# Kernel optimization log

Hardware: AMD Instinct MI355X
Metric: run time of the kernel (lower is better)

Reference implementation:

```python
import jax, jax.numpy as jnp
import numpy as np

DIM = 384
NUM_BLOCKS = 3
BATCH = 1024

def setup_inputs() -> dict:
    key = jax.random.key(0)
    k1, k2, kW, kL = jax.random.split(key, 4)
    v1 = jax.random.normal(k1, (BATCH, DIM), dtype=jnp.float32)
    v2 = jax.random.normal(k2, (BATCH, DIM), dtype=jnp.float32)
    block_W = jax.random.normal(kW, (NUM_BLOCKS, DIM, DIM), dtype=jnp.float32) * 0.02
    block_b = jnp.zeros((NUM_BLOCKS, DIM, DIM), dtype=jnp.float32)
    row_weights = jnp.ones((DIM,), dtype=jnp.float32) / DIM
    lim = 1.0 / np.sqrt(DIM)
    kLw, kLb = jax.random.split(kL)
    lin_W = jax.random.uniform(kLw, (DIM, DIM), minval=-lim, maxval=lim, dtype=jnp.float32)
    lin_b = jax.random.uniform(kLb, (DIM,), minval=-lim, maxval=lim, dtype=jnp.float32)
    return {"v1": v1, "v2": v2, "block_W": block_W, "block_b": block_b,
            "row_weights": row_weights, "lin_W": lin_W, "lin_b": lin_b}

def reference(v1, v2, block_W, block_b, row_weights, lin_W, lin_b):
    # outer product: (B, D, D)
    M = v1[:, :, None] * v2[:, None, :]
    for i in range(block_W.shape[0]):
        # M - (M*W + b) = M*(1 - W) - b, fused elementwise affine
        M = M * (1.0 - block_W[i]) - block_b[i]
    pooled = jnp.einsum('i,bij->bj', row_weights, M)
    # nn.Linear: x @ W.T + b
    return pooled @ lin_W.T + lin_b
```

## Files before the change

kernel.cpp:

```cpp
#include <hip/hip_runtime.h>
#include <hip/hip_bf16.h>

#define DIM 384
#define BATCH 1024
#define SPLANE (DIM * DIM)

__device__ __forceinline__ unsigned tobf(float x) {
    unsigned u = __float_as_uint(x);
    return (u + 0x7fffu + ((u >> 16) & 1u)) >> 16;
}
__device__ __forceinline__ float bflo(unsigned u) {
    return __uint_as_float(u << 16);
}
__device__ __forceinline__ float bfhi(unsigned u) {
    return __uint_as_float(u & 0xffff0000u);
}

__global__ __launch_bounds__(128)
void prep_kernel(const float* __restrict__ W,
                 const float* __restrict__ Bb,
                 const float* __restrict__ rw,
                 unsigned* __restrict__ Prwp,
                 float* __restrict__ qc) {
    const int j  = blockIdx.x * 128 + threadIdx.x;
    const int i0 = blockIdx.y * 6;
    float s = 0.0f;
    float p[6];
    #pragma unroll
    for (int ii = 0; ii < 6; ++ii) {
        const int i = i0 + ii;
        const int idx = i * DIM + j;
        float w0 = W[idx], w1 = W[SPLANE + idx], w2 = W[2 * SPLANE + idx];
        float b0 = Bb[idx], b1 = Bb[SPLANE + idx], b2 = Bb[2 * SPLANE + idx];
        float r1 = 1.0f - w1, r2 = 1.0f - w2;
        float r = rw[i];
        p[ii] = r * (1.0f - w0) * r1 * r2;
        s += r * (b0 * r1 * r2 + b1 * r2 + b2);
    }
    #pragma unroll
    for (int t = 0; t < 3; ++t) {
        unsigned lo = tobf(p[2 * t]);
        unsigned hi = tobf(p[2 * t + 1]);
        Prwp[(3 * blockIdx.y + t) * DIM + j] = lo | (hi << 16);
    }
    atomicAdd(&qc[j], s);
}

__global__ __launch_bounds__(256)
void tconv_kernel(const float* __restrict__ Wl,
                  unsigned* __restrict__ Wtp) {
    __shared__ float T[64][65];
    const int n0 = blockIdx.x * 64;
    const int j0 = blockIdx.y * 64;
    const int tid = threadIdx.x;
    const int c  = tid & 63;
    const int r4 = tid >> 6;
    #pragma unroll
    for (int q = 0; q < 16; ++q) {
        int row = r4 + 4 * q;
        T[row][c] = Wl[(n0 + row) * DIM + j0 + c];
    }
    __syncthreads();
    #pragma unroll
    for (int q = 0; q < 8; ++q) {
        int jp = r4 + 4 * q;
        unsigned lo = tobf(T[c][2 * jp]);
        unsigned hi = tobf(T[c][2 * jp + 1]);
        Wtp[(j0 / 2 + jp) * DIM + n0 + c] = lo | (hi << 16);
    }
}

__global__ __launch_bounds__(384)
void fused_kernel(const float* __restrict__ v1,
                  const float* __restrict__ v2,
                  const unsigned* __restrict__ Prwp,
                  const unsigned* __restrict__ Wtp,
                  const float* __restrict__ qc,
                  const float* __restrict__ lb,
                  float* __restrict__ out) {
    __shared__ float AT[DIM][4];
    __shared__ float PT[DIM][4];
    const int bm  = blockIdx.x * 4;
    const int tid = threadIdx.x;

    {
        const int r  = tid & 3;
        const int kq = tid >> 2;
        float4 a = *(const float4*)&v1[(bm + r) * DIM + 4 * kq];
        AT[4 * kq + 0][r] = a.x;
        AT[4 * kq + 1][r] = a.y;
        AT[4 * kq + 2][r] = a.z;
        AT[4 * kq + 3][r] = a.w;
    }
    __syncthreads();

    float a0 = 0.f, a1 = 0.f, a2 = 0.f, a3 = 0.f;
    {
        const unsigned* bp = Prwp + tid;
        #pragma unroll 8
        for (int kp = 0; kp < DIM / 2; ++kp) {
            unsigned u = bp[kp * DIM];
            float blo = bflo(u), bhi = bfhi(u);
            float4 va = *(const float4*)&AT[2 * kp][0];
            float4 vb = *(const float4*)&AT[2 * kp + 1][0];
            a0 += va.x * blo + vb.x * bhi;
            a1 += va.y * blo + vb.y * bhi;
            a2 += va.z * blo + vb.z * bhi;
            a3 += va.w * blo + vb.w * bhi;
        }
    }
    {
        float q = qc[tid];
        float4 pv;
        pv.x = v2[(bm + 0) * DIM + tid] * a0 - q;
        pv.y = v2[(bm + 1) * DIM + tid] * a1 - q;
        pv.z = v2[(bm + 2) * DIM + tid] * a2 - q;
        pv.w = v2[(bm + 3) * DIM + tid] * a3 - q;
        *(float4*)&PT[tid][0] = pv;
    }
    __syncthreads();

    float o0 = 0.f, o1 = 0.f, o2 = 0.f, o3 = 0.f;
    {
        const unsigned* wp = Wtp + tid;
        #pragma unroll 8
        for (int jp = 0; jp < DIM / 2; ++jp) {
            unsigned u = wp[jp * DIM];
            float wlo = bflo(u), whi = bfhi(u);
            float4 pa = *(const float4*)&PT[2 * jp][0];
            float4 pb = *(const float4*)&PT[2 * jp + 1][0];
            o0 += pa.x * wlo + pb.x * whi;
            o1 += pa.y * wlo + pb.y * whi;
            o2 += pa.z * wlo + pb.z * whi;
            o3 += pa.w * wlo + pb.w * whi;
        }
    }
    {
        float b = lb[tid];
        out[(bm + 0) * DIM + tid] = o0 + b;
        out[(bm + 1) * DIM + tid] = o1 + b;
        out[(bm + 2) * DIM + tid] = o2 + b;
        out[(bm + 3) * DIM + tid] = o3 + b;
    }
}

extern "C" void kernel_launch(void* const* d_in, const int* in_sizes, int n_in,
                              void* d_out, int out_size, void* d_ws, size_t ws_size,
                              hipStream_t stream) {
    const float* v1  = (const float*)d_in[0];
    const float* v2  = (const float*)d_in[1];
    const float* bW  = (const float*)d_in[2];
    const float* bB  = (const float*)d_in[3];
    const float* rw  = (const float*)d_in[4];
    const float* lW  = (const float*)d_in[5];
    const float* lb  = (const float*)d_in[6];
    float* out = (float*)d_out;

    float*    qc   = (float*)d_ws;
    unsigned* Prwp = (unsigned*)((char*)d_ws + 4096);
    unsigned* Wtp  = Prwp + (DIM / 2) * DIM;

    hipMemsetAsync(qc, 0, DIM * sizeof(float), stream);

    dim3 gp(DIM / 128, DIM / 6);
    prep_kernel<<<gp, 128, 0, stream>>>(bW, bB, rw, Prwp, qc);

    dim3 gt(DIM / 64, DIM / 64);
    tconv_kernel<<<gt, 256, 0, stream>>>(lW, Wtp);

    fused_kernel<<<BATCH / 4, 384, 0, stream>>>(v1, v2, Prwp, Wtp, qc, lb, out);
}
```

Baseline: 99.83 us.

## Merge prep kernels, drop memset and atomics, widen bf16 weight loads to uint2

Combines the block-weight precompute and the linear-weight transpose/convert into one launch, and removes the memset plus atomicAdd by writing per-block partial bias sums that the main kernel reduces itself. Weights are repacked as four bf16 values per uint2, so the GEMV loops issue half as many global loads, each twice as wide. This trades two launches and a memset for a 96-element partial-sum reduction inside every fused block.

Result: no change. 101.6 us (+1.8%).

```diff
diff --git a/kernel.cpp b/kernel.cpp
--- a/kernel.cpp
+++ b/kernel.cpp
@@ -9,73 +9,73 @@
     unsigned u = __float_as_uint(x);
     return (u + 0x7fffu + ((u >> 16) & 1u)) >> 16;
 }
-__device__ __forceinline__ float bflo(unsigned u) {
-    return __uint_as_float(u << 16);
-}
-__device__ __forceinline__ float bfhi(unsigned u) {
-    return __uint_as_float(u & 0xffff0000u);
-}
+__device__ __forceinline__ float bflo(unsigned u) { return __uint_as_float(u << 16); }
+__device__ __forceinline__ float bfhi(unsigned u) { return __uint_as_float(u & 0xffff0000u); }
 
-__global__ __launch_bounds__(128)
-void prep_kernel(const float* __restrict__ W,
-                 const float* __restrict__ Bb,
-                 const float* __restrict__ rw,
-                 unsigned* __restrict__ Prwp,
-                 float* __restrict__ qc) {
-    const int j  = blockIdx.x * 128 + threadIdx.x;
-    const int i0 = blockIdx.y * 6;
-    float s = 0.0f;
-    float p[6];
-    #pragma unroll
-    for (int ii = 0; ii < 6; ++ii) {
-        const int i = i0 + ii;
-        const int idx = i * DIM + j;
-        float w0 = W[idx], w1 = W[SPLANE + idx], w2 = W[2 * SPLANE + idx];
-        float b0 = Bb[idx], b1 = Bb[SPLANE + idx], b2 = Bb[2 * SPLANE + idx];
-        float r1 = 1.0f - w1, r2 = 1.0f - w2;
-        float r = rw[i];
-        p[ii] = r * (1.0f - w0) * r1 * r2;
-        s += r * (b0 * r1 * r2 + b1 * r2 + b2);
-    }
-    #pragma unroll
-    for (int t = 0; t < 3; ++t) {
-        unsigned lo = tobf(p[2 * t]);
-        unsigned hi = tobf(p[2 * t + 1]);
-        Prwp[(3 * blockIdx.y + t) * DIM + j] = lo | (hi << 16);
-    }
-    atomicAdd(&qc[j], s);
-}
+__global__ __launch_bounds__(384)
+void prep_all(const float* __restrict__ W,
+              const float* __restrict__ Bb,
+              const float* __restrict__ rw,
+              const float* __restrict__ Wl,
+              unsigned* __restrict__ Pq,
+              unsigned* __restrict__ Wtq,
+              float* __restrict__ qpart) {
+    __shared__ float T[96][65];
+    const int bx = blockIdx.x;
+    const int tid = threadIdx.x;
 
-__global__ __launch_bounds__(256)
-void tconv_kernel(const float* __restrict__ Wl,
-                  unsigned* __restrict__ Wtp) {
-    __shared__ float T[64][65];
-    const int n0 = blockIdx.x * 64;
-    const int j0 = blockIdx.y * 64;
-    const int tid = threadIdx.x;
-    const int c  = tid & 63;
-    const int r4 = tid >> 6;
-    #pragma unroll
-    for (int q = 0; q < 16; ++q) {
-        int row = r4 + 4 * q;
-        T[row][c] = Wl[(n0 + row) * DIM + j0 + c];
-    }
-    __syncthreads();
-    #pragma unroll
-    for (int q = 0; q < 8; ++q) {
-        int jp = r4 + 4 * q;
-        unsigned lo = tobf(T[c][2 * jp]);
-        unsigned hi = tobf(T[c][2 * jp + 1]);
-        Wtp[(j0 / 2 + jp) * DIM + n0 + c] = lo | (hi << 16);
+    if (bx < 96) {
+        const int i0 = bx * 4;
+        const int j  = tid;
+        float p[4];
+        float s = 0.0f;
+        #pragma unroll
+        for (int ii = 0; ii < 4; ++ii) {
+            const int i = i0 + ii;
+            const int idx = i * DIM + j;
+            float w0 = W[idx], w1 = W[SPLANE + idx], w2 = W[2 * SPLANE + idx];
+            float b0 = Bb[idx], b1 = Bb[SPLANE + idx], b2 = Bb[2 * SPLANE + idx];
+            float r1 = 1.0f - w1, r2 = 1.0f - w2;
+            float r = rw[i];
+            p[ii] = r * (1.0f - w0) * r1 * r2;
+            s += r * (b0 * r1 * r2 + b1 * r2 + b2);
+        }
+        uint2 u;
+        u.x = tobf(p[0]) | (tobf(p[1]) << 16);
+        u.y = tobf(p[2]) | (tobf(p[3]) << 16);
+        *(uint2*)&Pq[bx * 2 * DIM + 2 * j] = u;
+        qpart[bx * DIM + j] = s;
+    } else {
+        const int b  = bx - 96;
+        const int n0 = (b & 3) * 96;
+        const int j0 = (b >> 2) * 64;
+        const int c  = tid & 63;
+        const int r6 = tid >> 6;
+        #pragma unroll
+        for (int qq = 0; qq < 16; ++qq) {
+            int row = r6 + 6 * qq;
+            T[row][c] = Wl[(n0 + row) * DIM + j0 + c];
+        }
+        __syncthreads();
+        const int tn = tid % 96;
+        const int q4 = tid / 96;
+        #pragma unroll
+        for (int cc = 0; cc < 4; ++cc) {
+            int q = q4 + 4 * cc;
+            uint2 u;
+            u.x = tobf(T[tn][4 * q + 0]) | (tobf(T[tn][4 * q + 1]) << 16);
+            u.y = tobf(T[tn][4 * q + 2]) | (tobf(T[tn][4 * q + 3]) << 16);
+            *(uint2*)&Wtq[(j0 / 4 + q) * 2 * DIM + 2 * (n0 + tn)] = u;
+        }
     }
 }
 
 __global__ __launch_bounds__(384)
 void fused_kernel(const float* __restrict__ v1,
                   const float* __restrict__ v2,
-                  const unsigned* __restrict__ Prwp,
-                  const unsigned* __restrict__ Wtp,
-                  const float* __restrict__ qc,
+                  const unsigned* __restrict__ Pq,
+                  const unsigned* __restrict__ Wtq,
+                  const float* __restrict__ qpart,
                   const float* __restrict__ lb,
                   float* __restrict__ out) {
     __shared__ float AT[DIM][4];
@@ -92,47 +92,63 @@
         AT[4 * kq + 2][r] = a.z;
         AT[4 * kq + 3][r] = a.w;
     }
+
+    float q0 = 0.f, q1 = 0.f;
+    {
+        const float* qp = qpart + tid;
+        #pragma unroll 8
+        for (int p = 0; p < 96; p += 2) {
+            q0 += qp[p * DIM];
+            q1 += qp[(p + 1) * DIM];
+        }
+    }
+    const float qc = q0 + q1;
     __syncthreads();
 
     float a0 = 0.f, a1 = 0.f, a2 = 0.f, a3 = 0.f;
     {
-        const unsigned* bp = Prwp + tid;
+        const unsigned* bp = Pq + 2 * tid;
         #pragma unroll 8
-        for (int kp = 0; kp < DIM / 2; ++kp) {
-            unsigned u = bp[kp * DIM];
-            float blo = bflo(u), bhi = bfhi(u);
-            float4 va = *(const float4*)&AT[2 * kp][0];
-            float4 vb = *(const float4*)&AT[2 * kp + 1][0];
-            a0 += va.x * blo + vb.x * bhi;
-            a1 += va.y * blo + vb.y * bhi;
-            a2 += va.z * blo + vb.z * bhi;
-            a3 += va.w * blo + vb.w * bhi;
+        for (int kq = 0; kq < 96; ++kq) {
+            uint2 u = *(const uint2*)&bp[kq * 2 * DIM];
+            float b0 = bflo(u.x), b1 = bfhi(u.x);
+            float b2 = bflo(u.y), b3 = bfhi(u.y);
+            float4 va = *(const float4*)&AT[4 * kq + 0][0];
+            float4 vb = *(const float4*)&AT[4 * kq + 1][0];
+            float4 vc = *(const float4*)&AT[4 * kq + 2][0];
+            float4 vd = *(const float4*)&AT[4 * kq + 3][0];
+            a0 += va.x * b0 + vb.x * b1 + vc.x * b2 + vd.x * b3;
+            a1 += va.y * b0 + vb.y * b1 + vc.y * b2 + vd.y * b3;
+            a2 += va.z * b0 + vb.z * b1 + vc.z * b2 + vd.z * b3;
+            a3 += va.w * b0 + vb.w * b1 + vc.w * b2 + vd.w * b3;
         }
     }
     {
-        float q = qc[tid];
         float4 pv;
-        pv.x = v2[(bm + 0) * DIM + tid] * a0 - q;
-        pv.y = v2[(bm + 1) * DIM + tid] * a1 - q;
-        pv.z = v2[(bm + 2) * DIM + tid] * a2 - q;
-        pv.w = v2[(bm + 3) * DIM + tid] * a3 - q;
+        pv.x = v2[(bm + 0) * DIM + tid] * a0 - qc;
+        pv.y = v2[(bm + 1) * DIM + tid] * a1 - qc;
+        pv.z = v2[(bm + 2) * DIM + tid] * a2 - qc;
+        pv.w = v2[(bm + 3) * DIM + tid] * a3 - qc;
         *(float4*)&PT[tid][0] = pv;
     }
     __syncthreads();
 
     float o0 = 0.f, o1 = 0.f, o2 = 0.f, o3 = 0.f;
     {
-        const unsigned* wp = Wtp + tid;
+        const unsigned* wp = Wtq + 2 * tid;
         #pragma unroll 8
-        for (int jp = 0; jp < DIM / 2; ++jp) {
-            unsigned u = wp[jp * DIM];
-            float wlo = bflo(u), whi = bfhi(u);
-            float4 pa = *(const float4*)&PT[2 * jp][0];
-            float4 pb = *(const float4*)&PT[2 * jp + 1][0];
-            o0 += pa.x * wlo + pb.x * whi;
-            o1 += pa.y * wlo + pb.y * whi;
-            o2 += pa.z * wlo + pb.z * whi;
-            o3 += pa.w * wlo + pb.w * whi;
+        for (int jq = 0; jq < 96; ++jq) {
+            uint2 u = *(const uint2*)&wp[jq * 2 * DIM];
+            float b0 = bflo(u.x), b1 = bfhi(u.x);
+            float b2 = bflo(u.y), b3 = bfhi(u.y);
+            float4 pa = *(const float4*)&PT[4 * jq + 0][0];
+            float4 pb = *(const float4*)&PT[4 * jq + 1][0];
+            float4 pc = *(const float4*)&PT[4 * jq + 2][0];
+            float4 pd = *(const float4*)&PT[4 * jq + 3][0];
+            o0 += pa.x * b0 + pb.x * b1 + pc.x * b2 + pd.x * b3;
+            o1 += pa.y * b0 + pb.y * b1 + pc.y * b2 + pd.y * b3;
+            o2 += pa.z * b0 + pb.z * b1 + pc.z * b2 + pd.z * b3;
+            o3 += pa.w * b0 + pb.w * b1 + pc.w * b2 + pd.w * b3;
         }
     }
     {
@@ -156,17 +172,10 @@
     const float* lb  = (const float*)d_in[6];
     float* out = (float*)d_out;
 
-    float*    qc   = (float*)d_ws;
-    unsigned* Prwp = (unsigned*)((char*)d_ws + 4096);
-    unsigned* Wtp  = Prwp + (DIM / 2) * DIM;
+    unsigned* Pq    = (unsigned*)d_ws;
+    unsigned* Wtq   = Pq + (DIM / 4) * 2 * DIM;
+    float*    qpart = (float*)(Wtq + (DIM / 4) * 2 * DIM);
 
-    hipMemsetAsync(qc, 0, DIM * sizeof(float), stream);
-
-    dim3 gp(DIM / 128, DIM / 6);
-    prep_kernel<<<gp, 128, 0, stream>>>(bW, bB, rw, Prwp, qc);
-
-    dim3 gt(DIM / 64, DIM / 64);
-    tconv_kernel<<<gt, 256, 0, stream>>>(lW, Wtp);
-
-    fused_kernel<<<BATCH / 4, 384, 0, stream>>>(v1, v2, Prwp, Wtp, qc, lb, out);
+    prep_all<<<120, 384, 0, stream>>>(bW, bB, rw, lW, Pq, Wtq, qpart);
+    fused_kernel<<<BATCH / 4, 384, 0, stream>>>(v1, v2, Pq, Wtq, qpart, lb, out);
 }
```
